# Optimization experiments

Hardware: AMD Instinct MI355X
Metric: run time of the kernel (lower is better)

The kernel has to match this reference:

```python
import jax, jax.numpy as jnp
import numpy as np

H = 8       # num_heads
HD = 32     # transformer_head_dim
LN_EPS = 1e-5


def _layernorm(x, g, b):
    m = jnp.mean(x, axis=-1, keepdims=True)
    v = jnp.mean(jnp.square(x - m), axis=-1, keepdims=True)
    return (x - m) * jax.lax.rsqrt(v + LN_EPS) * g + b


def setup_inputs() -> dict:
    key = jax.random.key(0)
    ks = jax.random.split(key, 8)
    D, DFF = 256, 1024
    B, N = 8, 2048
    s = 0.02  # weight init scale
    return {
        "x": jax.random.normal(ks[0], (B, N, D), jnp.float32),
        "w_qkv": jax.random.normal(ks[1], (3 * H * HD, D), jnp.float32) * s,
        "w_out": jax.random.normal(ks[2], (D, H * HD), jnp.float32) * s,
        "b_out": jnp.zeros((D,), jnp.float32),
        "w1": jax.random.normal(ks[3], (DFF, D), jnp.float32) * s,
        "wv": jax.random.normal(ks[4], (DFF, D), jnp.float32) * s,
        "w2": jax.random.normal(ks[5], (D, DFF), jnp.float32) * s,
        "ln1_g": jnp.ones((D,), jnp.float32),
        "ln1_b": jnp.zeros((D,), jnp.float32),
        "ln2_g": jnp.ones((D,), jnp.float32),
        "ln2_b": jnp.zeros((D,), jnp.float32),
    }


def reference(x, w_qkv, w_out, b_out, w1, wv, w2, ln1_g, ln1_b, ln2_g, ln2_b):
    B, N, D = x.shape
    scale = HD ** (-0.5)
    # --- MultiHeadedAttention ---
    qkv = x @ w_qkv.T                                   # [B,N,3*H*HD]
    q, k, v = jnp.split(qkv, 3, axis=-1)
    def to_heads(t):
        return t.reshape(B, N, H, HD).transpose(0, 2, 1, 3)  # [B,H,N,HD]
    q, k, v = to_heads(q), to_heads(k), to_heads(v)
    sim = jnp.einsum("bhid,bhjd->bhij", q, k) * scale   # [B,H,N,N]
    attn = jax.nn.softmax(sim, axis=-1)
    o = jnp.einsum("bhij,bhjd->bhid", attn, v)
    o = o.transpose(0, 2, 1, 3).reshape(B, N, H * HD)
    y = o @ w_out.T + b_out                             # attn output
    # --- attn AddNorm: ln(dropout(y)+x), dropout off ---
    x1 = _layernorm(y + x, ln1_g, ln1_b)
    # --- GEGLU FFN applied to y (faithful to source) ---
    ff = jax.nn.gelu(y @ w1.T, approximate=False) * (y @ wv.T)
    ff = ff @ w2.T
    # --- ff AddNorm ---
    return _layernorm(ff + x1, ln2_g, ln2_b)
```

## Files before the change

### kernel.cpp

```cpp
#include <hip/hip_runtime.h>

typedef unsigned short u16;
typedef __bf16 bf16;
typedef __bf16 bf16x8 __attribute__((ext_vector_type(8)));
typedef __bf16 bf16x4 __attribute__((ext_vector_type(4)));
typedef short s16x4 __attribute__((ext_vector_type(4)));
typedef float f32x4 __attribute__((ext_vector_type(4)));
typedef unsigned short u16x8 __attribute__((ext_vector_type(8)));
typedef unsigned short u16x4 __attribute__((ext_vector_type(4)));
typedef unsigned short u16x2 __attribute__((ext_vector_type(2)));

#define DEVI static __device__ __forceinline__

DEVI float bf2f(u16 h) { return __builtin_bit_cast(float, (unsigned)h << 16); }
DEVI u16 cvt_bf(float f) { return __builtin_bit_cast(u16, (bf16)f); }

DEVI void gload16(const u16* g, u16* l) {
  __builtin_amdgcn_global_load_lds(
      (const __attribute__((address_space(1))) void*)g,
      (__attribute__((address_space(3))) void*)l, 16, 0, 0);
}

DEVI float gelu_exact(float x) {
  return 0.5f * x * (1.0f + erff(x * 0.70710678118654752f));
}

DEVI f32x4 mfma16(bf16x4 a, bf16x4 b, f32x4 c) {
#if __has_builtin(__builtin_amdgcn_mfma_f32_16x16x16bf16_1k)
  return __builtin_amdgcn_mfma_f32_16x16x16bf16_1k(
      __builtin_bit_cast(s16x4, a), __builtin_bit_cast(s16x4, b), c, 0, 0, 0);
#else
  f32x4 r = c;
  asm volatile("s_nop 1\n\tv_mfma_f32_16x16x16_bf16 %0, %1, %2, %0\n\ts_nop 7\n\ts_nop 3"
               : "+v"(r) : "v"(a), "v"(b));
  return r;
#endif
}

__global__ __launch_bounds__(256) void k_cast(const float* __restrict__ x,
                                              const float* __restrict__ wqkv,
                                              const float* __restrict__ wout,
                                              const float* __restrict__ w1,
                                              const float* __restrict__ wv,
                                              const float* __restrict__ w2,
                                              u16* __restrict__ dst0) {
  long i = (long)blockIdx.x * 256 + threadIdx.x;
  const float* src;
  u16* dst;
  long off;
  if (i < 1048576)       { src = x;    dst = dst0;           off = i; }
  else if (i < 1097728)  { src = wqkv; dst = dst0 + 4194304; off = i - 1048576; }
  else if (i < 1114112)  { src = wout; dst = dst0 + 4390912; off = i - 1097728; }
  else if (i < 1179648)  { src = w1;   dst = dst0 + 4456448; off = i - 1114112; }
  else if (i < 1245184)  { src = wv;   dst = dst0 + 4718592; off = i - 1179648; }
  else                   { src = w2;   dst = dst0 + 4980736; off = i - 1245184; }
  float4 f = reinterpret_cast<const float4*>(src)[off];
  u16x4 o;
  o[0] = cvt_bf(f.x); o[1] = cvt_bf(f.y); o[2] = cvt_bf(f.z); o[3] = cvt_bf(f.w);
  reinterpret_cast<u16x4*>(dst)[off] = o;
}

template <int BM, int BN, int NI>
__global__ __launch_bounds__(256) void k_gemm(const u16* __restrict__ A, const u16* __restrict__ B0,
                                              const u16* __restrict__ B1, int Nsplit,
                                              const float* __restrict__ bias,
                                              u16* __restrict__ C, int N, int K) {
  constexpr int MI = BM / 32;
  constexpr int ASZ = BM * 64, BSZ = BN * 64;
  __shared__ u16 Alds[2 * ASZ];
  __shared__ u16 Blds[2 * BSZ];
  const int m0 = blockIdx.x * BM;
  const int n0 = blockIdx.y * BN;
  const u16* Ap = A + (long)m0 * K;
  const u16* Bp = (n0 < Nsplit) ? (B0 + (long)n0 * K) : (B1 + (long)(n0 - Nsplit) * K);
  const int tid = threadIdx.x, lane = tid & 63, wave = tid >> 6;
  const int wr = (wave >> 1) * (BM / 2), wc = (wave & 1) * (BN / 2);
  const int lr = lane & 15, g = lane >> 4;
  const int sr = lane >> 3, sg = lane & 7;

  auto stage = [&](int kt, int buf) {
    const int kb = kt << 6;
#pragma unroll
    for (int c = 0; c < BM / 32; ++c) {
      const int row = wave * (BM / 4) + c * 8 + sr;
      gload16(Ap + (long)row * K + kb + ((sg ^ (row & 7)) << 3),
              &Alds[buf * ASZ + ((wave * (BM / 4) + c * 8) << 6)]);
    }
#pragma unroll
    for (int c = 0; c < BN / 32; ++c) {
      const int row = wave * (BN / 4) + c * 8 + sr;
      gload16(Bp + (long)row * K + kb + ((sg ^ ((row / NI) & 7)) << 3),
              &Blds[buf * BSZ + ((wave * (BN / 4) + c * 8) << 6)]);
    }
  };

  f32x4 acc[MI][NI] = {};
  const int nk = K >> 6;
  stage(0, 0);
  for (int kt = 0; kt < nk; ++kt) {
    const int ab = (kt & 1) * ASZ, bb = (kt & 1) * BSZ;
    __syncthreads();
    if (kt + 1 < nk) stage(kt + 1, (kt + 1) & 1);
#pragma unroll
    for (int kk = 0; kk < 2; ++kk) {
      bf16x8 av[MI], bv[NI];
#pragma unroll
      for (int i = 0; i < MI; ++i) {
        const int ra = wr + i * 16 + lr;
        av[i] = *reinterpret_cast<const bf16x8*>(&Alds[ab + (ra << 6) + (((kk * 4 + g) ^ (ra & 7)) << 3)]);
      }
#pragma unroll
      for (int ni = 0; ni < NI; ++ni) {
        const int rb = wc + lr * NI + ni;
        bv[ni] = *reinterpret_cast<const bf16x8*>(&Blds[bb + (rb << 6) + (((kk * 4 + g) ^ ((rb / NI) & 7)) << 3)]);
      }
#pragma unroll
      for (int mi = 0; mi < MI; ++mi)
#pragma unroll
        for (int ni = 0; ni < NI; ++ni)
          acc[mi][ni] = __builtin_amdgcn_mfma_f32_16x16x32_bf16(av[mi], bv[ni], acc[mi][ni], 0, 0, 0);
    }
  }
  const int colb = n0 + wc + lr * NI;
  float bvv[NI];
#pragma unroll
  for (int ni = 0; ni < NI; ++ni) bvv[ni] = bias ? bias[colb + ni] : 0.0f;
#pragma unroll
  for (int mi = 0; mi < MI; ++mi) {
#pragma unroll
    for (int r = 0; r < 4; ++r) {
      const long row = m0 + wr + mi * 16 + g * 4 + r;
      if constexpr (NI == 4) {
        u16x4 v;
#pragma unroll
        for (int ni = 0; ni < 4; ++ni) v[ni] = cvt_bf(acc[mi][ni][r] + bvv[ni]);
        *reinterpret_cast<u16x4*>(C + row * N + colb) = v;
      } else {
        u16x2 v;
#pragma unroll
        for (int ni = 0; ni < 2; ++ni) v[ni] = cvt_bf(acc[mi][ni][r] + bvv[ni]);
        *reinterpret_cast<u16x2*>(C + row * N + colb) = v;
      }
    }
  }
}

__global__ __launch_bounds__(256) void k_glu(const u16* __restrict__ A, const u16* __restrict__ W1,
                                             const u16* __restrict__ Wv, u16* __restrict__ C) {
  constexpr int K = 256, N = 1024;
  constexpr int ASZ = 128 * 64, BSZ = 64 * 64;
  __shared__ u16 Alds[2 * ASZ];
  __shared__ u16 Blds[2 * BSZ];
  const int m0 = blockIdx.x * 128;
  const int n0h = blockIdx.y * 32;
  const u16* Ap = A + (long)m0 * K;
  const int tid = threadIdx.x, lane = tid & 63, wave = tid >> 6;
  const int lr = lane & 15, g = lane >> 4;
  const int sr = lane >> 3, sg = lane & 7;

  auto stage = [&](int kt, int buf) {
    const int kb = kt << 6;
#pragma unroll
    for (int c = 0; c < 4; ++c) {
      const int row = wave * 32 + c * 8 + sr;
      gload16(Ap + (long)row * K + kb + ((sg ^ (row & 7)) << 3),
              &Alds[buf * ASZ + ((wave * 32 + c * 8) << 6)]);
    }
#pragma unroll
    for (int c = 0; c < 2; ++c) {
      const int row = wave * 16 + c * 8 + sr;
      const u16* bp = (row & 1) ? Wv : W1;
      gload16(bp + (long)(n0h + (row >> 1)) * K + kb + ((sg ^ ((row >> 2) & 7)) << 3),
              &Blds[buf * BSZ + ((wave * 16 + c * 8) << 6)]);
    }
  };

  f32x4 acc[2][4] = {};
  stage(0, 0);
  for (int kt = 0; kt < 4; ++kt) {
    const int ab = (kt & 1) * ASZ, bb = (kt & 1) * BSZ;
    __syncthreads();
    if (kt + 1 < 4) stage(kt + 1, (kt + 1) & 1);
#pragma unroll
    for (int kk = 0; kk < 2; ++kk) {
      bf16x8 av[2], bv[4];
#pragma unroll
      for (int i = 0; i < 2; ++i) {
        const int ra = wave * 32 + i * 16 + lr;
        av[i] = *reinterpret_cast<const bf16x8*>(&Alds[ab + (ra << 6) + (((kk * 4 + g) ^ (ra & 7)) << 3)]);
      }
#pragma unroll
      for (int ni = 0; ni < 4; ++ni) {
        const int rb = lr * 4 + ni;
        bv[ni] = *reinterpret_cast<const bf16x8*>(&Blds[bb + (rb << 6) + (((kk * 4 + g) ^ ((rb >> 2) & 7)) << 3)]);
      }
#pragma unroll
      for (int mi = 0; mi < 2; ++mi)
#pragma unroll
        for (int ni = 0; ni < 4; ++ni)
          acc[mi][ni] = __builtin_amdgcn_mfma_f32_16x16x32_bf16(av[mi], bv[ni], acc[mi][ni], 0, 0, 0);
    }
  }
  const int j0 = n0h + lr * 2;
#pragma unroll
  for (int mi = 0; mi < 2; ++mi) {
#pragma unroll
    for (int r = 0; r < 4; ++r) {
      const long row = m0 + wave * 32 + mi * 16 + g * 4 + r;
      u16x2 v;
      v[0] = cvt_bf(gelu_exact(acc[mi][0][r]) * acc[mi][1][r]);
      v[1] = cvt_bf(gelu_exact(acc[mi][2][r]) * acc[mi][3][r]);
      *reinterpret_cast<u16x2*>(C + row * N + j0) = v;
    }
  }
}

__global__ __launch_bounds__(256) void k_vt(const u16* __restrict__ qkv, u16* __restrict__ vt) {
  const int bh = blockIdx.x & 63, nt = blockIdx.x >> 6;
  const int b = bh >> 3, h = bh & 7;
  const int wave = threadIdx.x >> 6, lane = threadIdx.x & 63;
  const int dcol = wave * 8;
#pragma unroll
  for (int i = 0; i < 4; ++i) {
    const int nn = nt * 256 + i * 64 + lane;
    u16x8 v = *reinterpret_cast<const u16x8*>(qkv + (long)(b * 2048 + nn) * 768 + 512 + h * 32 + dcol);
#pragma unroll
    for (int j = 0; j < 8; ++j)
      vt[(long)(bh * 32 + dcol + j) * 2048 + nn] = v[j];
  }
}

__global__ __launch_bounds__(512) void k_attn(const u16* __restrict__ qkv, const u16* __restrict__ vt,
                                              u16* __restrict__ o) {
  __shared__ u16 Klds[2 * 4096];
  __shared__ u16 Vlds[2 * 4096];
  const int id = blockIdx.x;
  const int qt = id >> 6, bh = id & 63;
  const int b = bh >> 3, h = bh & 7;
  const int tid = threadIdx.x, wave = tid >> 6, lane = tid & 63;
  const int lq = lane & 15, g = lane >> 4, lqh = lq & 7;

  bf16x8 qf[2];
#pragma unroll
  for (int qi = 0; qi < 2; ++qi) {
    const long qrow = (long)(b * 2048 + qt * 256 + wave * 32 + qi * 16 + lq);
    const u16x8 qraw = *reinterpret_cast<const u16x8*>(qkv + qrow * 768 + h * 32 + g * 8);
#pragma unroll
    for (int j = 0; j < 8; ++j) qf[qi][j] = (bf16)(bf2f(qraw[j]) * 0.25503486f);
  }

  const int rK = tid >> 3, gpK = tid & 7, lK = gpK ^ (rK & 7);
  const u16* ksrc = qkv + (long)(b * 2048 + (lK >> 2) * 64 + rK) * 768 + 256 + h * 32 + (lK & 3) * 8;
  const int dV = tid >> 4, gpV = tid & 15, lgV = gpV ^ ((dV & 3) << 1);
  const u16* vsrc = vt + (long)(bh * 32 + dV) * 2048 + lgV * 8;
  u16* kdst = Klds + wave * 512;
  u16* vdst = Vlds + wave * 512;

  gload16(ksrc, kdst);
  gload16(vsrc, vdst);

  float m[2] = {-1e30f, -1e30f};
  f32x4 oacc[2][2] = {};
  f32x4 lacc[2] = {};
  const f32x4 zero = {0.0f, 0.0f, 0.0f, 0.0f};
  bf16x4 onesf;
  onesf[0] = onesf[1] = onesf[2] = onesf[3] = (bf16)1.0f;

  for (int kt = 0; kt < 16; ++kt) {
    const int bo = (kt & 1) * 4096;
    __syncthreads();
    if (kt + 1 < 16) {
      const int nbo = ((kt + 1) & 1) * 4096;
      gload16(ksrc + (long)(kt + 1) * 98304, kdst + nbo);
      gload16(vsrc + (kt + 1) * 128, vdst + nbo);
    }
    f32x4 s[2][8];
    __builtin_amdgcn_s_setprio(1);
#pragma unroll
    for (int f = 0; f < 8; ++f) {
      const bf16x8 kf = *reinterpret_cast<const bf16x8*>(
          &Klds[bo + (((f & 3) * 16 + lq) << 6) + ((((f >> 2) * 4 + g) ^ lqh) << 3)]);
      s[0][f] = __builtin_amdgcn_mfma_f32_16x16x32_bf16(kf, qf[0], zero, 0, 0, 0);
      s[1][f] = __builtin_amdgcn_mfma_f32_16x16x32_bf16(kf, qf[1], zero, 0, 0, 0);
    }
    __builtin_amdgcn_s_setprio(0);
#pragma unroll
    for (int qi = 0; qi < 2; ++qi) {
      float tmax = -1e30f;
#pragma unroll
      for (int f = 0; f < 8; ++f) {
        const float m01 = fmaxf(s[qi][f][0], s[qi][f][1]);
        const float m23 = fmaxf(s[qi][f][2], s[qi][f][3]);
        tmax = fmaxf(tmax, fmaxf(m01, m23));
      }
      if (__any(tmax > m[qi] + 8.0f)) {
        tmax = fmaxf(tmax, __shfl_xor(tmax, 16));
        tmax = fmaxf(tmax, __shfl_xor(tmax, 32));
        const float mnew = fmaxf(m[qi], tmax);
        const float alpha = exp2f(m[qi] - mnew);
#pragma unroll
        for (int di = 0; di < 2; ++di)
#pragma unroll
          for (int r = 0; r < 4; ++r) oacc[qi][di][r] *= alpha;
#pragma unroll
        for (int r = 0; r < 4; ++r) lacc[qi][r] *= alpha;
        m[qi] = mnew;
      }
#pragma unroll
      for (int f = 0; f < 8; ++f)
#pragma unroll
        for (int r = 0; r < 4; ++r) s[qi][f][r] = exp2f(s[qi][f][r] - m[qi]);
    }
    __builtin_amdgcn_s_setprio(1);
#pragma unroll
    for (int f = 0; f < 8; ++f) {
      const int gl8 = (f >> 2) * 16 + (f & 3) * 4 + g;
      const int ph8 = gl8 ^ ((lq & 3) << 2);
      bf16x4 vf[2];
#pragma unroll
      for (int di = 0; di < 2; ++di)
        vf[di] = *reinterpret_cast<const bf16x4*>(&Vlds[bo + (di * 16 + lq) * 128 + ph8 * 4]);
#pragma unroll
      for (int qi = 0; qi < 2; ++qi) {
        bf16x4 pf4;
        pf4[0] = (bf16)s[qi][f][0]; pf4[1] = (bf16)s[qi][f][1];
        pf4[2] = (bf16)s[qi][f][2]; pf4[3] = (bf16)s[qi][f][3];
        lacc[qi] = mfma16(onesf, pf4, lacc[qi]);
        oacc[qi][0] = mfma16(vf[0], pf4, oacc[qi][0]);
        oacc[qi][1] = mfma16(vf[1], pf4, oacc[qi][1]);
      }
    }
    __builtin_amdgcn_s_setprio(0);
  }

#pragma unroll
  for (int qi = 0; qi < 2; ++qi) {
    const float inv = 1.0f / lacc[qi][0];
    const long orow = (long)(b * 2048 + qt * 256 + wave * 32 + qi * 16 + lq);
#pragma unroll
    for (int di = 0; di < 2; ++di) {
      u16x4 ov;
#pragma unroll
      for (int r = 0; r < 4; ++r) ov[r] = cvt_bf(oacc[qi][di][r] * inv);
      *reinterpret_cast<u16x4*>(o + orow * 256 + h * 32 + di * 16 + g * 4) = ov;
    }
  }
}

__global__ __launch_bounds__(256) void k_ln(const u16* __restrict__ yin, const float* __restrict__ xres,
                                            const float* __restrict__ gw, const float* __restrict__ bw,
                                            float* __restrict__ out) {
  const int row = blockIdx.x * 4 + (threadIdx.x >> 6);
  const int lane = threadIdx.x & 63;
  const long base = (long)row * 256 + lane * 4;
  const float4 xv = *reinterpret_cast<const float4*>(xres + base);
  const u16x4 yv = *reinterpret_cast<const u16x4*>(yin + base);
  float s0 = bf2f(yv[0]) + xv.x;
  float s1 = bf2f(yv[1]) + xv.y;
  float s2 = bf2f(yv[2]) + xv.z;
  float s3 = bf2f(yv[3]) + xv.w;
  float sum = s0 + s1 + s2 + s3;
  float sq = s0 * s0 + s1 * s1 + s2 * s2 + s3 * s3;
#pragma unroll
  for (int msk = 1; msk < 64; msk <<= 1) {
    sum += __shfl_xor(sum, msk);
    sq += __shfl_xor(sq, msk);
  }
  const float mean = sum * (1.0f / 256.0f);
  const float var = sq * (1.0f / 256.0f) - mean * mean;
  const float rstd = rsqrtf(var + 1e-5f);
  const int c = lane * 4;
  float4 ov;
  ov.x = (s0 - mean) * rstd * gw[c + 0] + bw[c + 0];
  ov.y = (s1 - mean) * rstd * gw[c + 1] + bw[c + 1];
  ov.z = (s2 - mean) * rstd * gw[c + 2] + bw[c + 2];
  ov.w = (s3 - mean) * rstd * gw[c + 3] + bw[c + 3];
  *reinterpret_cast<float4*>(out + base) = ov;
}

extern "C" void kernel_launch(void* const* d_in, const int* in_sizes, int n_in,
                              void* d_out, int out_size, void* d_ws, size_t ws_size,
                              hipStream_t stream) {
  (void)in_sizes; (void)n_in; (void)out_size;
  if (ws_size < 136314880ULL) return;

  const float* x     = (const float*)d_in[0];
  const float* w_qkv = (const float*)d_in[1];
  const float* w_out = (const float*)d_in[2];
  const float* b_out = (const float*)d_in[3];
  const float* w1    = (const float*)d_in[4];
  const float* wv    = (const float*)d_in[5];
  const float* w2    = (const float*)d_in[6];
  const float* ln1g  = (const float*)d_in[7];
  const float* ln1b  = (const float*)d_in[8];
  const float* ln2g  = (const float*)d_in[9];
  const float* ln2b  = (const float*)d_in[10];
  float* outp = (float*)d_out;

  char* ws = (char*)d_ws;
  u16* xb    = (u16*)ws;
  u16* wqkvb = xb + 4194304;
  u16* woutb = wqkvb + 196608;
  u16* w1b   = woutb + 65536;
  u16* wvb   = w1b + 262144;
  u16* w2b   = wvb + 262144;
  u16* qkvb  = w2b + 262144;
  u16* ob    = qkvb + 12582912;
  u16* yb    = ob + 4194304;
  float* x1  = (float*)(ws + 52428800);
  u16* vtb   = (u16*)(ws + 69206016);
  u16* ffin  = qkvb;
  u16* ff2   = xb;

  k_cast<<<5120, 256, 0, stream>>>(x, w_qkv, w_out, w1, wv, w2, xb);
  k_gemm<128, 128, 4><<<dim3(128, 6), 256, 0, stream>>>(xb, wqkvb, wqkvb, 1 << 30, nullptr, qkvb, 768, 256);
  k_vt<<<512, 256, 0, stream>>>(qkvb, vtb);
  k_attn<<<512, 512, 0, stream>>>(qkvb, vtb, ob);
  k_gemm<128, 64, 2><<<dim3(128, 4), 256, 0, stream>>>(ob, woutb, woutb, 1 << 30, b_out, yb, 256, 256);
  k_ln<<<4096, 256, 0, stream>>>(yb, x, ln1g, ln1b, x1);
  k_glu<<<dim3(128, 32), 256, 0, stream>>>(yb, w1b, wvb, ffin);
  k_gemm<128, 64, 2><<<dim3(128, 4), 256, 0, stream>>>(ffin, w2b, w2b, 1 << 30, nullptr, ff2, 256, 1024);
  k_ln<<<4096, 256, 0, stream>>>(ff2, x1, ln2g, ln2b, outp);
}
```

Baseline: 286.9 us.

## Drop LDS staging in attention; load K/V fragments directly from global

```diff
diff --git a/kernel.cpp b/kernel.cpp
--- a/kernel.cpp
+++ b/kernel.cpp
@@ -230,120 +230,102 @@
   }
 }
 
-__global__ __launch_bounds__(512) void k_attn(const u16* __restrict__ qkv, const u16* __restrict__ vt,
+__global__ __launch_bounds__(256) void k_attn(const u16* __restrict__ qkv, const u16* __restrict__ vt,
                                               u16* __restrict__ o) {
-  __shared__ u16 Klds[2 * 4096];
-  __shared__ u16 Vlds[2 * 4096];
   const int id = blockIdx.x;
   const int qt = id >> 6, bh = id & 63;
   const int b = bh >> 3, h = bh & 7;
   const int tid = threadIdx.x, wave = tid >> 6, lane = tid & 63;
-  const int lq = lane & 15, g = lane >> 4, lqh = lq & 7;
-
-  bf16x8 qf[2];
-#pragma unroll
-  for (int qi = 0; qi < 2; ++qi) {
-    const long qrow = (long)(b * 2048 + qt * 256 + wave * 32 + qi * 16 + lq);
-    const u16x8 qraw = *reinterpret_cast<const u16x8*>(qkv + qrow * 768 + h * 32 + g * 8);
-#pragma unroll
-    for (int j = 0; j < 8; ++j) qf[qi][j] = (bf16)(bf2f(qraw[j]) * 0.25503486f);
-  }
-
-  const int rK = tid >> 3, gpK = tid & 7, lK = gpK ^ (rK & 7);
-  const u16* ksrc = qkv + (long)(b * 2048 + (lK >> 2) * 64 + rK) * 768 + 256 + h * 32 + (lK & 3) * 8;
-  const int dV = tid >> 4, gpV = tid & 15, lgV = gpV ^ ((dV & 3) << 1);
-  const u16* vsrc = vt + (long)(bh * 32 + dV) * 2048 + lgV * 8;
-  u16* kdst = Klds + wave * 512;
-  u16* vdst = Vlds + wave * 512;
-
-  gload16(ksrc, kdst);
-  gload16(vsrc, vdst);
-
-  float m[2] = {-1e30f, -1e30f};
-  f32x4 oacc[2][2] = {};
-  f32x4 lacc[2] = {};
+  const int lq = lane & 15, g = lane >> 4;
+
+  const long qrow = (long)(b * 2048 + qt * 64 + wave * 16 + lq);
+  const u16x8 qraw = *reinterpret_cast<const u16x8*>(qkv + qrow * 768 + h * 32 + g * 8);
+  bf16x8 qf;
+#pragma unroll
+  for (int j = 0; j < 8; ++j) qf[j] = (bf16)(bf2f(qraw[j]) * 0.25503486f);
+
+  const u16* kptr = qkv + (long)(b * 2048 + lq) * 768 + 256 + h * 32 + g * 8;
+  const u16* vptr = vt + (long)(bh * 32 + lq) * 2048 + g * 4;
+
+  float m = -1e30f;
+  f32x4 oacc[2] = {};
+  f32x4 lacc = {};
   const f32x4 zero = {0.0f, 0.0f, 0.0f, 0.0f};
   bf16x4 onesf;
   onesf[0] = onesf[1] = onesf[2] = onesf[3] = (bf16)1.0f;
 
-  for (int kt = 0; kt < 16; ++kt) {
-    const int bo = (kt & 1) * 4096;
-    __syncthreads();
-    if (kt + 1 < 16) {
-      const int nbo = ((kt + 1) & 1) * 4096;
-      gload16(ksrc + (long)(kt + 1) * 98304, kdst + nbo);
-      gload16(vsrc + (kt + 1) * 128, vdst + nbo);
-    }
-    f32x4 s[2][8];
+  auto loadK = [&](bf16x8 (&kf)[4], int kt) {
+#pragma unroll
+    for (int f = 0; f < 4; ++f)
+      kf[f] = *reinterpret_cast<const bf16x8*>(kptr + (long)(kt * 64 + f * 16) * 768);
+  };
+
+  auto body = [&](bf16x8 (&kc)[4], bf16x8 (&kn)[4], int kt) {
+    if (kt + 1 < 32) loadK(kn, kt + 1);
+    bf16x4 vf[2][4];
+#pragma unroll
+    for (int f = 0; f < 4; ++f)
+#pragma unroll
+      for (int di = 0; di < 2; ++di)
+        vf[di][f] = *reinterpret_cast<const bf16x4*>(vptr + (long)(di * 16) * 2048 + kt * 64 + f * 16);
+    f32x4 s[4];
     __builtin_amdgcn_s_setprio(1);
 #pragma unroll
-    for (int f = 0; f < 8; ++f) {
-      const bf16x8 kf = *reinterpret_cast<const bf16x8*>(
-          &Klds[bo + (((f & 3) * 16 + lq) << 6) + ((((f >> 2) * 4 + g) ^ lqh) << 3)]);
-      s[0][f] = __builtin_amdgcn_mfma_f32_16x16x32_bf16(kf, qf[0], zero, 0, 0, 0);
-      s[1][f] = __builtin_amdgcn_mfma_f32_16x16x32_bf16(kf, qf[1], zero, 0, 0, 0);
-    }
+    for (int f = 0; f < 4; ++f)
+      s[f] = __builtin_amdgcn_mfma_f32_16x16x32_bf16(kc[f], qf, zero, 0, 0, 0);
     __builtin_amdgcn_s_setprio(0);
-#pragma unroll
-    for (int qi = 0; qi < 2; ++qi) {
-      float tmax = -1e30f;
-#pragma unroll
-      for (int f = 0; f < 8; ++f) {
-        const float m01 = fmaxf(s[qi][f][0], s[qi][f][1]);
-        const float m23 = fmaxf(s[qi][f][2], s[qi][f][3]);
-        tmax = fmaxf(tmax, fmaxf(m01, m23));
-      }
-      if (__any(tmax > m[qi] + 8.0f)) {
-        tmax = fmaxf(tmax, __shfl_xor(tmax, 16));
-        tmax = fmaxf(tmax, __shfl_xor(tmax, 32));
-        const float mnew = fmaxf(m[qi], tmax);
-        const float alpha = exp2f(m[qi] - mnew);
-#pragma unroll
-        for (int di = 0; di < 2; ++di)
-#pragma unroll
-          for (int r = 0; r < 4; ++r) oacc[qi][di][r] *= alpha;
-#pragma unroll
-        for (int r = 0; r < 4; ++r) lacc[qi][r] *= alpha;
-        m[qi] = mnew;
-      }
-#pragma unroll
-      for (int f = 0; f < 8; ++f)
-#pragma unroll
-        for (int r = 0; r < 4; ++r) s[qi][f][r] = exp2f(s[qi][f][r] - m[qi]);
-    }
+    float tmax = -1e30f;
+#pragma unroll
+    for (int f = 0; f < 4; ++f) {
+      const float m01 = fmaxf(s[f][0], s[f][1]);
+      const float m23 = fmaxf(s[f][2], s[f][3]);
+      tmax = fmaxf(tmax, fmaxf(m01, m23));
+    }
+    if (__any(tmax > m + 8.0f)) {
+      tmax = fmaxf(tmax, __shfl_xor(tmax, 16));
+      tmax = fmaxf(tmax, __shfl_xor(tmax, 32));
+      const float mnew = fmaxf(m, tmax);
+      const float alpha = exp2f(m - mnew);
+#pragma unroll
+      for (int di = 0; di < 2; ++di)
+#pragma unroll
+        for (int r = 0; r < 4; ++r) oacc[di][r] *= alpha;
+#pragma unroll
+      for (int r = 0; r < 4; ++r) lacc[r] *= alpha;
+      m = mnew;
+    }
+#pragma unroll
+    for (int f = 0; f < 4; ++f)
+#pragma unroll
+      for (int r = 0; r < 4; ++r) s[f][r] = exp2f(s[f][r] - m);
     __builtin_amdgcn_s_setprio(1);
 #pragma unroll
-    for (int f = 0; f < 8; ++f) {
-      const int gl8 = (f >> 2) * 16 + (f & 3) * 4 + g;
-      const int ph8 = gl8 ^ ((lq & 3) << 2);
-      bf16x4 vf[2];
-#pragma unroll
-      for (int di = 0; di < 2; ++di)
-        vf[di] = *reinterpret_cast<const bf16x4*>(&Vlds[bo + (di * 16 + lq) * 128 + ph8 * 4]);
-#pragma unroll
-      for (int qi = 0; qi < 2; ++qi) {
-        bf16x4 pf4;
-        pf4[0] = (bf16)s[qi][f][0]; pf4[1] = (bf16)s[qi][f][1];
-        pf4[2] = (bf16)s[qi][f][2]; pf4[3] = (bf16)s[qi][f][3];
-        lacc[qi] = mfma16(onesf, pf4, lacc[qi]);
-        oacc[qi][0] = mfma16(vf[0], pf4, oacc[qi][0]);
-        oacc[qi][1] = mfma16(vf[1], pf4, oacc[qi][1]);
-      }
+    for (int f = 0; f < 4; ++f) {
+      bf16x4 pf4;
+      pf4[0] = (bf16)s[f][0]; pf4[1] = (bf16)s[f][1];
+      pf4[2] = (bf16)s[f][2]; pf4[3] = (bf16)s[f][3];
+      lacc = mfma16(onesf, pf4, lacc);
+      oacc[0] = mfma16(vf[0][f], pf4, oacc[0]);
+      oacc[1] = mfma16(vf[1][f], pf4, oacc[1]);
     }
     __builtin_amdgcn_s_setprio(0);
-  }
-
-#pragma unroll
-  for (int qi = 0; qi < 2; ++qi) {
-    const float inv = 1.0f / lacc[qi][0];
-    const long orow = (long)(b * 2048 + qt * 256 + wave * 32 + qi * 16 + lq);
-#pragma unroll
-    for (int di = 0; di < 2; ++di) {
-      u16x4 ov;
-#pragma unroll
-      for (int r = 0; r < 4; ++r) ov[r] = cvt_bf(oacc[qi][di][r] * inv);
-      *reinterpret_cast<u16x4*>(o + orow * 256 + h * 32 + di * 16 + g * 4) = ov;
-    }
+  };
+
+  bf16x8 kA[4], kB[4];
+  loadK(kA, 0);
+  for (int kt2 = 0; kt2 < 16; ++kt2) {
+    body(kA, kB, 2 * kt2);
+    body(kB, kA, 2 * kt2 + 1);
+  }
+
+  const float inv = 1.0f / lacc[0];
+  const long orow = (long)(b * 2048 + qt * 64 + wave * 16 + lq);
+#pragma unroll
+  for (int di = 0; di < 2; ++di) {
+    u16x4 ov;
+#pragma unroll
+    for (int r = 0; r < 4; ++r) ov[r] = cvt_bf(oacc[di][r] * inv);
+    *reinterpret_cast<u16x4*>(o + orow * 256 + h * 32 + di * 16 + g * 4) = ov;
   }
 }
 
@@ -415,7 +397,7 @@
   k_cast<<<5120, 256, 0, stream>>>(x, w_qkv, w_out, w1, wv, w2, xb);
   k_gemm<128, 128, 4><<<dim3(128, 6), 256, 0, stream>>>(xb, wqkvb, wqkvb, 1 << 30, nullptr, qkvb, 768, 256);
   k_vt<<<512, 256, 0, stream>>>(qkvb, vtb);
-  k_attn<<<512, 512, 0, stream>>>(qkvb, vtb, ob);
+  k_attn<<<2048, 256, 0, stream>>>(qkvb, vtb, ob);
   k_gemm<128, 64, 2><<<dim3(128, 4), 256, 0, stream>>>(ob, woutb, woutb, 1 << 30, b_out, yb, 256, 256);
   k_ln<<<4096, 256, 0, stream>>>(yb, x, ln1g, ln1b, x1);
   k_glu<<<dim3(128, 32), 256, 0, stream>>>(yb, w1b, wvb, ffin);
```

Result: slower. 513.1 us (+78.8%).
